# Kernel tuning notes

Hardware: AMD Instinct MI355X
Metric: run time of the kernel (lower is better)

The kernel has to match this reference:

```python
import jax, jax.numpy as jnp
import numpy as np

D_MODEL = 4096
NUM_EXPERTS = 64


def setup_inputs() -> dict:
    key = jax.random.key(0)
    kx, kw, kb = jax.random.split(key, 3)
    x = jax.random.normal(kx, (4, 4096, D_MODEL), dtype=jnp.float32)
    # nn.Linear(d_model, num_experts): weight [E, D], bias [E]
    bound = 1.0 / np.sqrt(D_MODEL)
    W = jax.random.uniform(kw, (NUM_EXPERTS, D_MODEL), dtype=jnp.float32, minval=-bound, maxval=bound)
    b = jax.random.uniform(kb, (NUM_EXPERTS,), dtype=jnp.float32, minval=-bound, maxval=bound)
    return {"x": x, "W": W, "b": b}


def reference(x, W, b):
    # logits: [B, S, E]
    logits = jnp.einsum('bsd,ed->bse', x, W) + b
    scores = jax.nn.softmax(logits, axis=-1)
    val, idx = jax.lax.top_k(scores, 2)            # [B, S, 2]
    # scatter top-2 values back into a dense [B, S, E] dispatch mask
    onehot = jax.nn.one_hot(idx, NUM_EXPERTS, dtype=scores.dtype)  # [B, S, 2, E]
    dispatch = jnp.einsum('bsk,bske->bse', val, onehot)
    combine = dispatch
    expert_counts = dispatch.sum(axis=(0, 1))      # [E]
    return dispatch, combine, expert_counts
```

## Files before the change

### kernel.cpp

```cpp
#include <hip/hip_runtime.h>
#include <math.h>

#define D_MODEL 4096
#define NEXP    64
#define NTOK    16384
#define KSPLIT  16
#define KS      256
#define BMT     256

typedef __attribute__((ext_vector_type(8))) short  bf16x8;
typedef __attribute__((ext_vector_type(4))) float  f32x4;

__device__ __forceinline__ unsigned short f2bf_rn(float f) {
    union { float f; unsigned u; } v; v.f = f;
    unsigned r = v.u + 0x7fffu + ((v.u >> 16) & 1u);
    return (unsigned short)(r >> 16);
}
__device__ __forceinline__ float bf2f(unsigned short h) {
    union { unsigned u; float f; } v; v.u = ((unsigned)h) << 16;
    return v.f;
}
__device__ __forceinline__ void split2(float f0, float f1, unsigned& hw, unsigned& lw) {
    unsigned short h0 = f2bf_rn(f0), h1 = f2bf_rn(f1);
    unsigned short l0 = f2bf_rn(f0 - bf2f(h0)), l1 = f2bf_rn(f1 - bf2f(h1));
    hw = (unsigned)h0 | ((unsigned)h1 << 16);
    lw = (unsigned)l0 | ((unsigned)l1 << 16);
}

__global__ __launch_bounds__(256)
void k0_prep(const float* __restrict__ W, unsigned short* __restrict__ ws,
             float* __restrict__ logits, float* __restrict__ out) {
    const int gid = blockIdx.x * 256 + threadIdx.x;
    if (blockIdx.x == 0 && threadIdx.x < NEXP)
        out[(size_t)2 * NTOK * NEXP + threadIdx.x] = 0.f;
    float4 z = make_float4(0.f, 0.f, 0.f, 0.f);
    float* lz = logits + (size_t)gid * 16;
#pragma unroll
    for (int k = 0; k < 4; ++k)
        *reinterpret_cast<float4*>(&lz[k * 4]) = z;
    int i = gid * 4;
    float4 v = *reinterpret_cast<const float4*>(&W[i]);
    unsigned short h[4], l[4];
    float f[4] = {v.x, v.y, v.z, v.w};
#pragma unroll
    for (int k = 0; k < 4; ++k) {
        h[k] = f2bf_rn(f[k]);
        l[k] = f2bf_rn(f[k] - bf2f(h[k]));
    }
    *reinterpret_cast<short4*>(&ws[i])                  = make_short4(h[0], h[1], h[2], h[3]);
    *reinterpret_cast<short4*>(&ws[NEXP * D_MODEL + i]) = make_short4(l[0], l[1], l[2], l[3]);
}

__global__ __launch_bounds__(512, 4)
void k1_gemm(const float* __restrict__ x, const unsigned short* __restrict__ wsplit,
             float* __restrict__ logits) {
    __shared__ uint4 whi[NEXP * 32];
    __shared__ uint4 wlo[NEXP * 32];

    const int tid = threadIdx.x;
    const int t0  = (blockIdx.x >> 3) * BMT;
    const int sp  = blockIdx.x & 7;

    const int lane = tid & 63;
    const int rowl = lane & 15;
    const int grp  = lane >> 4;
    const int wtok = t0 + (tid >> 6) * 32;

    f32x4 acc[2][4];
#pragma unroll
    for (int m = 0; m < 2; ++m)
#pragma unroll
        for (int n = 0; n < 4; ++n)
            acc[m][n] = (f32x4){0.f, 0.f, 0.f, 0.f};

    for (int half = 0; half < 2; ++half) {
        const int ks0 = (sp * 2 + half) * KS;
        if (half) __syncthreads();

#pragma unroll
        for (int i = 0; i < 4; ++i) {
            int p  = tid + i * 512;
            int e  = p >> 5;
            int c  = p & 31;
            int cs = (c & 24) | ((c & 7) ^ (e & 7));
            const unsigned short* src = wsplit + (size_t)e * D_MODEL + ks0 + c * 8;
            whi[e * 32 + cs] = *reinterpret_cast<const uint4*>(src);
            wlo[e * 32 + cs] = *reinterpret_cast<const uint4*>(src + NEXP * D_MODEL);
        }
        __syncthreads();

        const float* xp0 = x + (size_t)(wtok + rowl) * D_MODEL + ks0 + grp * 8;
        const float* xp1 = xp0 + (size_t)16 * D_MODEL;

#pragma unroll
        for (int kb = 0; kb < 8; ++kb) {
            union { bf16x8 v; unsigned u[4]; } ah0, al0, ah1, al1;
            {
                f32x4 c0 = *reinterpret_cast<const f32x4*>(xp0 + kb * 32);
                f32x4 c1 = *reinterpret_cast<const f32x4*>(xp0 + kb * 32 + 4);
                split2(c0.x, c0.y, ah0.u[0], al0.u[0]);
                split2(c0.z, c0.w, ah0.u[1], al0.u[1]);
                split2(c1.x, c1.y, ah0.u[2], al0.u[2]);
                split2(c1.z, c1.w, ah0.u[3], al0.u[3]);
            }
            {
                f32x4 c0 = *reinterpret_cast<const f32x4*>(xp1 + kb * 32);
                f32x4 c1 = *reinterpret_cast<const f32x4*>(xp1 + kb * 32 + 4);
                split2(c0.x, c0.y, ah1.u[0], al1.u[0]);
                split2(c0.z, c0.w, ah1.u[1], al1.u[1]);
                split2(c1.x, c1.y, ah1.u[2], al1.u[2]);
                split2(c1.z, c1.w, ah1.u[3], al1.u[3]);
            }
            const int c  = kb * 4 + grp;
            const int cs = (c & 24) | ((c & 7) ^ (rowl & 7));
#pragma unroll
            for (int n = 0; n < 4; ++n) {
                const int idx = (n * 16 + rowl) * 32 + cs;
                bf16x8 bh = *reinterpret_cast<const bf16x8*>(&whi[idx]);
                bf16x8 bl = *reinterpret_cast<const bf16x8*>(&wlo[idx]);
                acc[0][n] = __builtin_amdgcn_mfma_f32_16x16x32_bf16(ah0.v, bh, acc[0][n], 0, 0, 0);
                acc[0][n] = __builtin_amdgcn_mfma_f32_16x16x32_bf16(ah0.v, bl, acc[0][n], 0, 0, 0);
                acc[0][n] = __builtin_amdgcn_mfma_f32_16x16x32_bf16(al0.v, bh, acc[0][n], 0, 0, 0);
                acc[1][n] = __builtin_amdgcn_mfma_f32_16x16x32_bf16(ah1.v, bh, acc[1][n], 0, 0, 0);
                acc[1][n] = __builtin_amdgcn_mfma_f32_16x16x32_bf16(ah1.v, bl, acc[1][n], 0, 0, 0);
                acc[1][n] = __builtin_amdgcn_mfma_f32_16x16x32_bf16(al1.v, bh, acc[1][n], 0, 0, 0);
            }
        }
    }

#pragma unroll
    for (int m = 0; m < 2; ++m)
#pragma unroll
        for (int n = 0; n < 4; ++n)
#pragma unroll
            for (int i = 0; i < 4; ++i) {
                const int t = wtok + m * 16 + grp * 4 + i;
                const int e = n * 16 + rowl;
                atomicAdd(&logits[(size_t)t * NEXP + e], acc[m][n][i]);
            }
}

__global__ __launch_bounds__(256)
void k2_softmax_top2(const float* __restrict__ logits, const float* __restrict__ bias,
                     float* __restrict__ out) {
    const int t = blockIdx.x * 256 + threadIdx.x;
    __shared__ float cnt[NEXP];
    __shared__ float bs[NEXP];
    if (threadIdx.x < NEXP) {
        cnt[threadIdx.x] = 0.f;
        bs[threadIdx.x]  = bias[threadIdx.x];
    }
    __syncthreads();

    float l[NEXP];
    const float* lp = logits + (size_t)t * NEXP;
#pragma unroll
    for (int g = 0; g < 16; ++g) {
        float4 v = *reinterpret_cast<const float4*>(&lp[g * 4]);
        l[4 * g + 0] = v.x + bs[4 * g + 0];
        l[4 * g + 1] = v.y + bs[4 * g + 1];
        l[4 * g + 2] = v.z + bs[4 * g + 2];
        l[4 * g + 3] = v.w + bs[4 * g + 3];
    }

    float m = l[0];
#pragma unroll
    for (int e = 1; e < NEXP; ++e) m = fmaxf(m, l[e]);

    float sum = 0.f;
#pragma unroll
    for (int e = 0; e < NEXP; ++e) sum += __expf(l[e] - m);

    float v1 = -INFINITY, v2 = -INFINITY;
    int   i1 = 0, i2 = 0;
#pragma unroll
    for (int e = 0; e < NEXP; ++e) {
        if (l[e] > v1) { v2 = v1; i2 = i1; v1 = l[e]; i1 = e; }
        else if (l[e] > v2) { v2 = l[e]; i2 = e; }
    }
    const float inv = 1.f / sum;
    const float s1 = __expf(v1 - m) * inv;
    const float s2 = __expf(v2 - m) * inv;

    float* disp = out + (size_t)t * NEXP;
    float* comb = out + (size_t)NTOK * NEXP + (size_t)t * NEXP;
#pragma unroll
    for (int g = 0; g < 16; ++g) {
        float4 o = make_float4(0.f, 0.f, 0.f, 0.f);
        if ((i1 >> 2) == g) (&o.x)[i1 & 3] = s1;
        if ((i2 >> 2) == g) (&o.x)[i2 & 3] = s2;
        *reinterpret_cast<float4*>(&disp[g * 4]) = o;
        *reinterpret_cast<float4*>(&comb[g * 4]) = o;
    }

    atomicAdd(&cnt[i1], s1);
    atomicAdd(&cnt[i2], s2);
    __syncthreads();
    if (threadIdx.x < NEXP)
        atomicAdd(&out[(size_t)2 * NTOK * NEXP + threadIdx.x], cnt[threadIdx.x]);
}

extern "C" void kernel_launch(void* const* d_in, const int* in_sizes, int n_in,
                              void* d_out, int out_size, void* d_ws, size_t ws_size,
                              hipStream_t stream) {
    const float* x = (const float*)d_in[0];
    const float* W = (const float*)d_in[1];
    const float* b = (const float*)d_in[2];
    float* out = (float*)d_out;
    unsigned short* ws = (unsigned short*)d_ws;
    float* logits = (float*)(ws + 2 * NEXP * D_MODEL);

    k0_prep<<<256, 256, 0, stream>>>(W, ws, logits, out);
    k1_gemm<<<(NTOK / BMT) * (KSPLIT / 2), 512, 0, stream>>>(x, ws, logits);
    k2_softmax_top2<<<NTOK / 256, 256, 0, stream>>>(logits, b, out);
}
```

Baseline: 89.16 us.

## Replace split-K atomic accumulation with per-split partial buffers reduced in softmax

Each K-split block of the GEMM now writes its partial logits to its own buffer with plain stores instead of issuing float atomicAdds into one shared logits array. The softmax kernel sums the eight partials per token before the bias, softmax and top-2 steps. This also removes the zeroing of the logits buffer in the prep kernel, and the softmax kernel now uses 128-thread blocks. The cost is about 8x more intermediate traffic (8 x 4 MB written and then read back) in place of atomic contention, plus a larger workspace requirement.

```diff
diff --git a/kernel.cpp b/kernel.cpp
--- a/kernel.cpp
+++ b/kernel.cpp
@@ -4,7 +4,7 @@
 #define D_MODEL 4096
 #define NEXP    64
 #define NTOK    16384
-#define KSPLIT  16
+#define NSP     8
 #define KS      256
 #define BMT     256
 
@@ -29,15 +29,10 @@
 
 __global__ __launch_bounds__(256)
 void k0_prep(const float* __restrict__ W, unsigned short* __restrict__ ws,
-             float* __restrict__ logits, float* __restrict__ out) {
+             float* __restrict__ out) {
     const int gid = blockIdx.x * 256 + threadIdx.x;
     if (blockIdx.x == 0 && threadIdx.x < NEXP)
         out[(size_t)2 * NTOK * NEXP + threadIdx.x] = 0.f;
-    float4 z = make_float4(0.f, 0.f, 0.f, 0.f);
-    float* lz = logits + (size_t)gid * 16;
-#pragma unroll
-    for (int k = 0; k < 4; ++k)
-        *reinterpret_cast<float4*>(&lz[k * 4]) = z;
     int i = gid * 4;
     float4 v = *reinterpret_cast<const float4*>(&W[i]);
     unsigned short h[4], l[4];
@@ -53,7 +48,7 @@
 
 __global__ __launch_bounds__(512, 4)
 void k1_gemm(const float* __restrict__ x, const unsigned short* __restrict__ wsplit,
-             float* __restrict__ logits) {
+             float* __restrict__ parts) {
     __shared__ uint4 whi[NEXP * 32];
     __shared__ uint4 wlo[NEXP * 32];
 
@@ -128,6 +123,7 @@
         }
     }
 
+    float* part = parts + (size_t)sp * NTOK * NEXP;
 #pragma unroll
     for (int m = 0; m < 2; ++m)
 #pragma unroll
@@ -136,14 +132,14 @@
             for (int i = 0; i < 4; ++i) {
                 const int t = wtok + m * 16 + grp * 4 + i;
                 const int e = n * 16 + rowl;
-                atomicAdd(&logits[(size_t)t * NEXP + e], acc[m][n][i]);
-            }
-}
-
-__global__ __launch_bounds__(256)
-void k2_softmax_top2(const float* __restrict__ logits, const float* __restrict__ bias,
+                part[(size_t)t * NEXP + e] = acc[m][n][i];
+            }
+}
+
+__global__ __launch_bounds__(128)
+void k2_softmax_top2(const float* __restrict__ parts, const float* __restrict__ bias,
                      float* __restrict__ out) {
-    const int t = blockIdx.x * 256 + threadIdx.x;
+    const int t = blockIdx.x * 128 + threadIdx.x;
     __shared__ float cnt[NEXP];
     __shared__ float bs[NEXP];
     if (threadIdx.x < NEXP) {
@@ -153,14 +149,19 @@
     __syncthreads();
 
     float l[NEXP];
-    const float* lp = logits + (size_t)t * NEXP;
+    const float* lp = parts + (size_t)t * NEXP;
 #pragma unroll
     for (int g = 0; g < 16; ++g) {
-        float4 v = *reinterpret_cast<const float4*>(&lp[g * 4]);
-        l[4 * g + 0] = v.x + bs[4 * g + 0];
-        l[4 * g + 1] = v.y + bs[4 * g + 1];
-        l[4 * g + 2] = v.z + bs[4 * g + 2];
-        l[4 * g + 3] = v.w + bs[4 * g + 3];
+        float4 a = *reinterpret_cast<const float4*>(&lp[g * 4]);
+#pragma unroll
+        for (int s = 1; s < NSP; ++s) {
+            float4 v = *reinterpret_cast<const float4*>(&lp[(size_t)s * NTOK * NEXP + g * 4]);
+            a.x += v.x; a.y += v.y; a.z += v.z; a.w += v.w;
+        }
+        l[4 * g + 0] = a.x + bs[4 * g + 0];
+        l[4 * g + 1] = a.y + bs[4 * g + 1];
+        l[4 * g + 2] = a.z + bs[4 * g + 2];
+        l[4 * g + 3] = a.w + bs[4 * g + 3];
     }
 
     float m = l[0];
@@ -208,9 +209,9 @@
     const float* b = (const float*)d_in[2];
     float* out = (float*)d_out;
     unsigned short* ws = (unsigned short*)d_ws;
-    float* logits = (float*)(ws + 2 * NEXP * D_MODEL);
-
-    k0_prep<<<256, 256, 0, stream>>>(W, ws, logits, out);
-    k1_gemm<<<(NTOK / BMT) * (KSPLIT / 2), 512, 0, stream>>>(x, ws, logits);
-    k2_softmax_top2<<<NTOK / 256, 256, 0, stream>>>(logits, b, out);
-}
+    float* parts = (float*)(ws + 2 * NEXP * D_MODEL);
+
+    k0_prep<<<256, 256, 0, stream>>>(W, ws, out);
+    k1_gemm<<<(NTOK / BMT) * NSP, 512, 0, stream>>>(x, ws, parts);
+    k2_softmax_top2<<<NTOK / 128, 128, 0, stream>>>(parts, b, out);
+}
```

After: 101.8 us. +14.2%, slower.
